# Kernel tuning notes

Hardware: AMD Instinct MI355X
Metric: run time of the kernel (lower is better)

## Reference

```python
import jax, jax.numpy as jnp
import numpy as np

B, S, D, H = 4, 1024, 1024, 16
DK = D // H
EPS_LN = 1e-6

def setup_inputs() -> dict:
    key = jax.random.key(0)
    ks = jax.random.split(key, 16)
    sc = 1.0 / np.sqrt(D)
    inp = {}
    names = ['q_r','q_i','k_r','k_i','v_r','v_i']
    for i, n in enumerate(names):
        inp[n] = jax.random.normal(ks[i], (B, S, D), dtype=jnp.float32)
    wnames = ['wq_r','wq_i','wk_r','wk_i','wv_r','wv_i','wfc_r','wfc_i']
    for i, n in enumerate(wnames):
        inp[n] = jax.random.normal(ks[6 + i], (D, D), dtype=jnp.float32) * sc
    inp['gamma'] = jnp.ones((D,), dtype=jnp.float32)
    inp['beta'] = jnp.zeros((D,), dtype=jnp.float32)
    return inp

def _clinear(xr, xi, wr, wi):
    # complex (xr + i*xi) @ (wr + i*wi)^T, weights stored [out, in]
    r = xr @ wr.T - xi @ wi.T
    im = xi @ wr.T + xr @ wi.T
    return r, im

def _forward(q_r, q_i, k_r, k_i, v_r, v_i, wq_r, wq_i, wk_r, wk_i,
             wv_r, wv_i, wfc_r, wfc_i, gamma, beta):
    res_r, res_i = q_r, q_i
    qr, qi = _clinear(q_r, q_i, wq_r, wq_i)
    kr, ki = _clinear(k_r, k_i, wk_r, wk_i)
    vr, vi = _clinear(v_r, v_i, wv_r, wv_i)
    # [B,S,D] -> [B,H,S,DK]
    split = lambda x: x.reshape(B, S, H, DK).transpose(0, 2, 1, 3)
    qr, qi, kr, ki, vr, vi = map(split, (qr, qi, kr, ki, vr, vi))
    temp = jnp.asarray(DK ** 0.5, qr.dtype)
    qr = qr / temp
    qi = qi / temp
    # q @ conj(k)^T : real = qr.kr + qi.ki ; imag = qi.kr - qr.ki
    ar = jnp.einsum('bhqd,bhkd->bhqk', qr, kr) + jnp.einsum('bhqd,bhkd->bhqk', qi, ki)
    ai = jnp.einsum('bhqd,bhkd->bhqk', qi, kr) - jnp.einsum('bhqd,bhkd->bhqk', qr, ki)
    attn = jax.nn.softmax(jnp.sqrt(ar * ar + ai * ai), axis=-1)  # magnitude softmax
    or_ = jnp.einsum('bhqk,bhkd->bhqd', attn, vr)
    oi_ = jnp.einsum('bhqk,bhkd->bhqd', attn, vi)
    merge = lambda x: x.transpose(0, 2, 1, 3).reshape(B, S, D)
    or_, oi_ = merge(or_), merge(oi_)
    fr, fi = _clinear(or_, oi_, wfc_r, wfc_i)
    # ComplexDropout in eval mode: identity except imag += 1e-10
    fi = fi + 1e-10
    xr = fr + res_r
    xi = fi + res_i
    # ComplexLayerNorm: mean over all non-batch dims, elementwise magnitude norm
    mr = jnp.mean(xr, axis=(1, 2), keepdims=True)
    mi = jnp.mean(xi, axis=(1, 2), keepdims=True)
    cr = xr - mr
    ci = xi - mi
    std = jnp.sqrt(cr * cr + ci * ci + EPS_LN)
    yr = gamma * (cr / std) + beta
    yi = gamma * (ci / std)
    return yr, yi, attn

def reference(q_r, q_i, k_r, k_i, v_r, v_i, wq_r, wq_i, wk_r, wk_i,
              wv_r, wv_i, wfc_r, wfc_i, gamma, beta):
    return _forward(q_r, q_i, k_r, k_i, v_r, v_i, wq_r, wq_i, wk_r, wk_i,
                    wv_r, wv_i, wfc_r, wfc_i, gamma, beta)
```

## Files before the change

kernel.cpp:

```cpp
#include <hip/hip_runtime.h>
#include <math.h>

#define NB 4
#define SEQ 1024
#define DIM 1024
#define NH 16
#define DHEAD 64
#define BUFN 4194304ULL
#define WHN  1048576ULL
#define LOG2E 1.4426950408889634f

typedef _Float16 f16x8 __attribute__((ext_vector_type(8)));
typedef _Float16 f16x4 __attribute__((ext_vector_type(4)));
typedef float    f32x4 __attribute__((ext_vector_type(4)));

#define MFMA16 __builtin_amdgcn_mfma_f32_16x16x32_f16

__device__ __forceinline__ void split4(const float4 v, f16x4& h, f16x4& l)
{
    const _Float16 h0=(_Float16)v.x, h1=(_Float16)v.y, h2=(_Float16)v.z, h3=(_Float16)v.w;
    h = (f16x4){h0, h1, h2, h3};
    l = (f16x4){(_Float16)((v.x-(float)h0)*2048.0f),
                (_Float16)((v.y-(float)h1)*2048.0f),
                (_Float16)((v.z-(float)h2)*2048.0f),
                (_Float16)((v.w-(float)h3)*2048.0f)};
}

__global__ __launch_bounds__(256)
void splitx_kernel(const float* __restrict__ xr, const float* __restrict__ xi,
                   _Float16* __restrict__ XS)
{
    const float* x = blockIdx.y ? xi : xr;
    _Float16* h = XS + (size_t)blockIdx.y * 2 * BUFN;
    _Float16* l = h + BUFN;
    const int i = (blockIdx.x * 256 + threadIdx.x) << 2;
    const float4 v = *(const float4*)(x + i);
    f16x4 hh, ll; split4(v, hh, ll);
    *(f16x4*)(h + i) = hh;
    *(f16x4*)(l + i) = ll;
}

__global__ __launch_bounds__(256)
void splitw_kernel(const float* w0, const float* w1, const float* w2, const float* w3,
                   const float* w4, const float* w5, const float* w6, const float* w7,
                   _Float16* __restrict__ WS)
{
    const int y = blockIdx.y;
    const float* x = (y==0)?w0:(y==1)?w1:(y==2)?w2:(y==3)?w3:(y==4)?w4:(y==5)?w5:(y==6)?w6:w7;
    _Float16* h = WS + (size_t)y * 2 * WHN;
    _Float16* l = h + WHN;
    const int i = (blockIdx.x * 256 + threadIdx.x) << 2;
    float4 v = *(const float4*)(x + i);
    v.x *= 64.0f; v.y *= 64.0f; v.z *= 64.0f; v.w *= 64.0f;
    f16x4 hh, ll; split4(v, hh, ll);
    *(f16x4*)(h + i) = hh;
    *(f16x4*)(l + i) = ll;
}

template<int MODE>
__global__ __launch_bounds__(256, 1)
void cgemm16_kernel(const _Float16* __restrict__ Ahr, const _Float16* __restrict__ Alr,
                    const _Float16* __restrict__ Ahi, const _Float16* __restrict__ Ali,
                    const _Float16* __restrict__ Bhr, const _Float16* __restrict__ Blr,
                    const _Float16* __restrict__ Bhi, const _Float16* __restrict__ Bli,
                    float* __restrict__ outr, float* __restrict__ outi,
                    const float* __restrict__ resr, const float* __restrict__ resi,
                    float* __restrict__ msum, float scale)
{
    __shared__ __align__(16) _Float16 As[4][64][40];
    __shared__ __align__(16) _Float16 Bs[4][64][40];
    const int t    = threadIdx.x;
    const int lane = t & 63;
    const int w    = t >> 6;
    const int wm   = w >> 1, wn = w & 1;
    const int lr   = lane & 15;
    const int kc   = (lane >> 4) << 3;
    const int m0   = blockIdx.x * 64;
    const int o0   = blockIdx.y * 64;
    const int srow = t >> 2;
    const int sc8  = (t & 3) << 3;

    const size_t aoff = (size_t)(m0 + srow) * DIM + sc8;
    const size_t boff = (size_t)(o0 + srow) * DIM + sc8;

    f32x4 acc[2][2][4];
    #pragma unroll
    for (int i = 0; i < 2; ++i)
        #pragma unroll
        for (int j = 0; j < 2; ++j)
            #pragma unroll
            for (int c = 0; c < 4; ++c)
                acc[i][j][c] = (f32x4){0.f, 0.f, 0.f, 0.f};

    for (int k0 = 0; k0 < DIM; k0 += 32) {
        const uint4 va0 = *(const uint4*)(Ahr + aoff + k0);
        const uint4 va1 = *(const uint4*)(Alr + aoff + k0);
        const uint4 va2 = *(const uint4*)(Ahi + aoff + k0);
        const uint4 va3 = *(const uint4*)(Ali + aoff + k0);
        const uint4 vb0 = *(const uint4*)(Bhr + boff + k0);
        const uint4 vb1 = *(const uint4*)(Blr + boff + k0);
        const uint4 vb2 = *(const uint4*)(Bhi + boff + k0);
        const uint4 vb3 = *(const uint4*)(Bli + boff + k0);
        __syncthreads();
        *(uint4*)&As[0][srow][sc8] = va0;
        *(uint4*)&As[1][srow][sc8] = va1;
        *(uint4*)&As[2][srow][sc8] = va2;
        *(uint4*)&As[3][srow][sc8] = va3;
        *(uint4*)&Bs[0][srow][sc8] = vb0;
        *(uint4*)&Bs[1][srow][sc8] = vb1;
        *(uint4*)&Bs[2][srow][sc8] = vb2;
        *(uint4*)&Bs[3][srow][sc8] = vb3;
        __syncthreads();

        f16x8 a0[2], a1[2], a2[2], a3[2];
        #pragma unroll
        for (int mt = 0; mt < 2; ++mt) {
            const int ar = wm * 32 + mt * 16 + lr;
            a0[mt] = *(const f16x8*)&As[0][ar][kc];
            a1[mt] = *(const f16x8*)&As[1][ar][kc];
            a2[mt] = *(const f16x8*)&As[2][ar][kc];
            a3[mt] = *(const f16x8*)&As[3][ar][kc];
        }
        #pragma unroll
        for (int nt = 0; nt < 2; ++nt) {
            const int br = wn * 32 + nt * 16 + lr;
            const f16x8 bhr = *(const f16x8*)&Bs[0][br][kc];
            const f16x8 blr = *(const f16x8*)&Bs[1][br][kc];
            const f16x8 bhi = *(const f16x8*)&Bs[2][br][kc];
            const f16x8 bli = *(const f16x8*)&Bs[3][br][kc];
            const f16x8 bhiN = -bhi;
            const f16x8 bliN = -bli;
            #pragma unroll
            for (int mt = 0; mt < 2; ++mt) {
                acc[mt][nt][0] = MFMA16(a0[mt], bhr,  acc[mt][nt][0], 0, 0, 0);
                acc[mt][nt][0] = MFMA16(a2[mt], bhiN, acc[mt][nt][0], 0, 0, 0);
                acc[mt][nt][1] = MFMA16(a0[mt], blr,  acc[mt][nt][1], 0, 0, 0);
                acc[mt][nt][1] = MFMA16(a1[mt], bhr,  acc[mt][nt][1], 0, 0, 0);
                acc[mt][nt][1] = MFMA16(a2[mt], bliN, acc[mt][nt][1], 0, 0, 0);
                acc[mt][nt][1] = MFMA16(a3[mt], bhiN, acc[mt][nt][1], 0, 0, 0);
                acc[mt][nt][2] = MFMA16(a2[mt], bhr,  acc[mt][nt][2], 0, 0, 0);
                acc[mt][nt][2] = MFMA16(a0[mt], bhi,  acc[mt][nt][2], 0, 0, 0);
                acc[mt][nt][3] = MFMA16(a2[mt], blr,  acc[mt][nt][3], 0, 0, 0);
                acc[mt][nt][3] = MFMA16(a3[mt], bhr,  acc[mt][nt][3], 0, 0, 0);
                acc[mt][nt][3] = MFMA16(a0[mt], bli,  acc[mt][nt][3], 0, 0, 0);
                acc[mt][nt][3] = MFMA16(a1[mt], bhi,  acc[mt][nt][3], 0, 0, 0);
            }
        }
    }

    const float INVL = 1.0f / 2048.0f;
    if (MODE == 0) {
        #pragma unroll
        for (int mt = 0; mt < 2; ++mt)
            #pragma unroll
            for (int nt = 0; nt < 2; ++nt)
                #pragma unroll
                for (int r = 0; r < 4; ++r) {
                    const int mrow = m0 + wm * 32 + mt * 16 + ((lane >> 4)) * 4 + r;
                    const int ncol = o0 + wn * 32 + nt * 16 + lr;
                    const float cr = (acc[mt][nt][0][r] + acc[mt][nt][1][r] * INVL) * scale;
                    const float ci = (acc[mt][nt][2][r] + acc[mt][nt][3][r] * INVL) * scale;
                    const int b = mrow >> 10, s = mrow & 1023, h = ncol >> 6, dk = ncol & 63;
                    const size_t idx = (((size_t)b * NH + h) * SEQ + s) * DHEAD + dk;
                    outr[idx] = cr;
                    outi[idx] = ci;
                }
    } else {
        float sr = 0.f, si = 0.f;
        #pragma unroll
        for (int mt = 0; mt < 2; ++mt)
            #pragma unroll
            for (int nt = 0; nt < 2; ++nt)
                #pragma unroll
                for (int r = 0; r < 4; ++r) {
                    const int mrow = m0 + wm * 32 + mt * 16 + ((lane >> 4)) * 4 + r;
                    const int ncol = o0 + wn * 32 + nt * 16 + lr;
                    const size_t idx = (size_t)mrow * DIM + ncol;
                    const float cr = (acc[mt][nt][0][r] + acc[mt][nt][1][r] * INVL) * scale
                                     + resr[idx];
                    const float ci = (acc[mt][nt][2][r] + acc[mt][nt][3][r] * INVL) * scale
                                     + 1e-10f + resi[idx];
                    outr[idx] = cr;
                    outi[idx] = ci;
                    sr += cr; si += ci;
                }
        #pragma unroll
        for (int off = 32; off > 0; off >>= 1) { sr += __shfl_xor(sr, off); si += __shfl_xor(si, off); }
        __shared__ float wsum[8];
        if ((t & 63) == 0) { wsum[w * 2 + 0] = sr; wsum[w * 2 + 1] = si; }
        __syncthreads();
        if (t == 0) {
            atomicAdd(&msum[2 * (m0 >> 10) + 0], wsum[0] + wsum[2] + wsum[4] + wsum[6]);
            atomicAdd(&msum[2 * (m0 >> 10) + 1], wsum[1] + wsum[3] + wsum[5] + wsum[7]);
        }
    }
}

__global__ __launch_bounds__(256)
void vtrans_kernel(const float* __restrict__ VR, const float* __restrict__ VI,
                   _Float16* __restrict__ Trh, _Float16* __restrict__ Trl,
                   _Float16* __restrict__ Tih, _Float16* __restrict__ Til)
{
    __shared__ float sr[64][68];
    __shared__ float si[64][68];
    const int t = threadIdx.x;
    const int kb = blockIdx.x, bh = blockIdx.y;
    const size_t ibase = (size_t)bh * SEQ * DHEAD + (size_t)kb * 64 * DHEAD;
    const int row = t >> 4, c0 = (t & 15) << 2;
    #pragma unroll
    for (int it = 0; it < 4; ++it) {
        const float4 a = *(const float4*)(VR + ibase + (size_t)(row + 16*it) * DHEAD + c0);
        const float4 b = *(const float4*)(VI + ibase + (size_t)(row + 16*it) * DHEAD + c0);
        *(float4*)&sr[row + 16*it][c0] = a;
        *(float4*)&si[row + 16*it][c0] = b;
    }
    __syncthreads();
    const int dk = t >> 2, k0 = (t & 3) << 4;
    f16x8 hr[2], lr8[2], hi8[2], li8[2];
    #pragma unroll
    for (int kk = 0; kk < 16; ++kk) {
        const float xr = sr[k0 + kk][dk];
        const float xi = si[k0 + kk][dk];
        const _Float16 hxr = (_Float16)xr;
        const _Float16 hxi = (_Float16)xi;
        hr[kk>>3][kk&7]  = hxr;
        lr8[kk>>3][kk&7] = (_Float16)((xr - (float)hxr) * 2048.0f);
        hi8[kk>>3][kk&7] = hxi;
        li8[kk>>3][kk&7] = (_Float16)((xi - (float)hxi) * 2048.0f);
    }
    const size_t ob = ((size_t)bh * 64 + dk) * SEQ + kb * 64 + k0;
    *(f16x8*)(Trh + ob) = hr[0];  *(f16x8*)(Trh + ob + 8) = hr[1];
    *(f16x8*)(Trl + ob) = lr8[0]; *(f16x8*)(Trl + ob + 8) = lr8[1];
    *(f16x8*)(Tih + ob) = hi8[0]; *(f16x8*)(Tih + ob + 8) = hi8[1];
    *(f16x8*)(Til + ob) = li8[0]; *(f16x8*)(Til + ob + 8) = li8[1];
}

__global__ __launch_bounds__(256, 1)
void attn_scores_kernel(const float* __restrict__ QR, const float* __restrict__ QI,
                        const float* __restrict__ KR, const float* __restrict__ KI,
                        float* __restrict__ attn, float* __restrict__ Lbuf)
{
    __shared__ __align__(16) _Float16 Ks[4][64][72];
    __shared__ float red[2][64];
    const int t = threadIdx.x;
    const int lane = t & 63;
    const int w = t >> 6, wm = w >> 1, wn = w & 1;
    const int lr = lane & 15, g = lane >> 4, kc = g << 3;
    const int q0 = blockIdx.x * 64;
    const int bh = blockIdx.y;
    const size_t base = (size_t)bh * SEQ * DHEAD;
    const int srow = t >> 2, sc0 = (t & 3) << 4;

    #pragma unroll
    for (int c = 0; c < 4; ++c) {
        const float4 a = *(const float4*)(QR + base + (size_t)(q0 + srow) * DHEAD + sc0 + 4*c);
        const float4 b = *(const float4*)(QI + base + (size_t)(q0 + srow) * DHEAD + sc0 + 4*c);
        f16x4 h, l;
        split4(a, h, l);
        *(f16x4*)&Ks[0][srow][sc0 + 4*c] = h;
        *(f16x4*)&Ks[1][srow][sc0 + 4*c] = l;
        split4(b, h, l);
        *(f16x4*)&Ks[2][srow][sc0 + 4*c] = h;
        *(f16x4*)&Ks[3][srow][sc0 + 4*c] = l;
    }
    __syncthreads();
    f16x8 qhr[2][2], qlr[2][2], qhi[2][2], qli[2][2];
    #pragma unroll
    for (int mt = 0; mt < 2; ++mt) {
        const int row = wm * 32 + mt * 16 + lr;
        #pragma unroll
        for (int ks = 0; ks < 2; ++ks) {
            const int col = ks * 32 + kc;
            qhr[mt][ks] = *(const f16x8*)&Ks[0][row][col];
            qlr[mt][ks] = *(const f16x8*)&Ks[1][row][col];
            qhi[mt][ks] = *(const f16x8*)&Ks[2][row][col];
            qli[mt][ks] = *(const f16x8*)&Ks[3][row][col];
        }
    }

    float lsum[2][4] = {};
    float4 pr[4], pi4[4];
    #pragma unroll
    for (int c = 0; c < 4; ++c) {
        pr[c]  = *(const float4*)(KR + base + (size_t)srow * DHEAD + sc0 + 4*c);
        pi4[c] = *(const float4*)(KI + base + (size_t)srow * DHEAD + sc0 + 4*c);
    }

    for (int kt = 0; kt < 16; ++kt) {
        __syncthreads();
        #pragma unroll
        for (int c = 0; c < 4; ++c) {
            f16x4 h, l;
            split4(pr[c], h, l);
            *(f16x4*)&Ks[0][srow][sc0 + 4*c] = h;
            *(f16x4*)&Ks[1][srow][sc0 + 4*c] = l;
            split4(pi4[c], h, l);
            *(f16x4*)&Ks[2][srow][sc0 + 4*c] = h;
            *(f16x4*)&Ks[3][srow][sc0 + 4*c] = l;
        }
        __syncthreads();
        if (kt < 15) {
            const size_t koff = base + (size_t)((kt + 1) * 64 + srow) * DHEAD;
            #pragma unroll
            for (int c = 0; c < 4; ++c) {
                pr[c]  = *(const float4*)(KR + koff + sc0 + 4*c);
                pi4[c] = *(const float4*)(KI + koff + sc0 + 4*c);
            }
        }
        f32x4 arh[2][2], arl[2][2], aih[2][2], ail[2][2];
        #pragma unroll
        for (int i = 0; i < 2; ++i)
            #pragma unroll
            for (int j = 0; j < 2; ++j) {
                arh[i][j] = (f32x4){0,0,0,0}; arl[i][j] = (f32x4){0,0,0,0};
                aih[i][j] = (f32x4){0,0,0,0}; ail[i][j] = (f32x4){0,0,0,0};
            }
        #pragma unroll
        for (int nt = 0; nt < 2; ++nt) {
            const int brow = wn * 32 + nt * 16 + lr;
            #pragma unroll
            for (int ks = 0; ks < 2; ++ks) {
                const int col = ks * 32 + kc;
                const f16x8 khr = *(const f16x8*)&Ks[0][brow][col];
                const f16x8 klr = *(const f16x8*)&Ks[1][brow][col];
                const f16x8 khi = *(const f16x8*)&Ks[2][brow][col];
                const f16x8 kli = *(const f16x8*)&Ks[3][brow][col];
                const f16x8 khiN = -khi;
                const f16x8 kliN = -kli;
                #pragma unroll
                for (int mt = 0; mt < 2; ++mt) {
                    arh[mt][nt] = MFMA16(qhr[mt][ks], khr,  arh[mt][nt], 0,0,0);
                    arh[mt][nt] = MFMA16(qhi[mt][ks], khi,  arh[mt][nt], 0,0,0);
                    arl[mt][nt] = MFMA16(qhr[mt][ks], klr,  arl[mt][nt], 0,0,0);
                    arl[mt][nt] = MFMA16(qlr[mt][ks], khr,  arl[mt][nt], 0,0,0);
                    arl[mt][nt] = MFMA16(qhi[mt][ks], kli,  arl[mt][nt], 0,0,0);
                    arl[mt][nt] = MFMA16(qli[mt][ks], khi,  arl[mt][nt], 0,0,0);
                    aih[mt][nt] = MFMA16(qhi[mt][ks], khr,  aih[mt][nt], 0,0,0);
                    aih[mt][nt] = MFMA16(qhr[mt][ks], khiN, aih[mt][nt], 0,0,0);
                    ail[mt][nt] = MFMA16(qhi[mt][ks], klr,  ail[mt][nt], 0,0,0);
                    ail[mt][nt] = MFMA16(qli[mt][ks], khr,  ail[mt][nt], 0,0,0);
                    ail[mt][nt] = MFMA16(qhr[mt][ks], kliN, ail[mt][nt], 0,0,0);
                    ail[mt][nt] = MFMA16(qlr[mt][ks], khiN, ail[mt][nt], 0,0,0);
                }
            }
        }
        const float INV = 1.0f / 2048.0f;
        #pragma unroll
        for (int mt = 0; mt < 2; ++mt)
            #pragma unroll
            for (int nt = 0; nt < 2; ++nt)
                #pragma unroll
                for (int r = 0; r < 4; ++r) {
                    const float ar = arh[mt][nt][r] + arl[mt][nt][r] * INV;
                    const float ai = aih[mt][nt][r] + ail[mt][nt][r] * INV;
                    const float s  = sqrtf(ar * ar + ai * ai);
                    const int q = q0 + wm * 32 + mt * 16 + g * 4 + r;
                    const int k = kt * 64 + wn * 32 + nt * 16 + lr;
                    attn[((size_t)bh * SEQ + q) * SEQ + k] = s;
                    lsum[mt][r] += exp2f(s * LOG2E);
                }
    }
    #pragma unroll
    for (int mt = 0; mt < 2; ++mt)
        #pragma unroll
        for (int r = 0; r < 4; ++r) {
            float v = lsum[mt][r];
            v += __shfl_xor(v, 1); v += __shfl_xor(v, 2);
            v += __shfl_xor(v, 4); v += __shfl_xor(v, 8);
            lsum[mt][r] = v;
        }
    if (lr == 0) {
        #pragma unroll
        for (int mt = 0; mt < 2; ++mt)
            #pragma unroll
            for (int r = 0; r < 4; ++r)
                red[wn][wm * 32 + mt * 16 + g * 4 + r] = lsum[mt][r];
    }
    __syncthreads();
    if (t < 64) Lbuf[(size_t)bh * SEQ + q0 + t] = red[0][t] + red[1][t];
}

__global__ __launch_bounds__(256, 1)
void attn_pv_kernel(float* __restrict__ attn, const float* __restrict__ Lbuf,
                    const _Float16* __restrict__ Trh, const _Float16* __restrict__ Trl,
                    const _Float16* __restrict__ Tih, const _Float16* __restrict__ Til,
                    _Float16* __restrict__ XOhr, _Float16* __restrict__ XOlr,
                    _Float16* __restrict__ XOhi, _Float16* __restrict__ XOli)
{
    __shared__ __align__(16) _Float16 Ps[2][64][72];
    __shared__ float invL[64];
    const int t = threadIdx.x;
    const int lane = t & 63;
    const int w = t >> 6, wm = w >> 1, wn = w & 1;
    const int lr = lane & 15, g = lane >> 4, kc = g << 3;
    const int q0 = blockIdx.x * 64;
    const int bh = blockIdx.y;
    const size_t abase = ((size_t)bh * SEQ + q0) * SEQ;
    const size_t vbase = (size_t)bh * 64 * SEQ;

    if (t < 64) invL[t] = 1.0f / Lbuf[(size_t)bh * SEQ + q0 + t];

    const size_t vrow[2] = { vbase + (size_t)(wn * 32 + lr) * SEQ + kc,
                             vbase + (size_t)(wn * 32 + 16 + lr) * SEQ + kc };

    f32x4 orh[2][2], orl[2][2], oih[2][2], oil[2][2];
    #pragma unroll
    for (int i = 0; i < 2; ++i)
        #pragma unroll
        for (int j = 0; j < 2; ++j) {
            orh[i][j] = (f32x4){0,0,0,0}; orl[i][j] = (f32x4){0,0,0,0};
            oih[i][j] = (f32x4){0,0,0,0}; oil[i][j] = (f32x4){0,0,0,0};
        }

    const int prow = t >> 4, pcol = (t & 15) << 2;
    float4 sc[4];
    #pragma unroll
    for (int it = 0; it < 4; ++it)
        sc[it] = *(const float4*)(attn + abase + (size_t)(prow + 16*it) * SEQ + pcol);

    for (int kt = 0; kt < 16; ++kt) {
        __syncthreads();
        #pragma unroll
        for (int it = 0; it < 4; ++it) {
            const int row = prow + 16*it;
            const float inv = invL[row];
            float4 p;
            p.x = exp2f(sc[it].x * LOG2E) * inv;
            p.y = exp2f(sc[it].y * LOG2E) * inv;
            p.z = exp2f(sc[it].z * LOG2E) * inv;
            p.w = exp2f(sc[it].w * LOG2E) * inv;
            *(float4*)(attn + abase + (size_t)row * SEQ + kt * 64 + pcol) = p;
            float4 ps;
            ps.x = p.x * 1024.0f; ps.y = p.y * 1024.0f;
            ps.z = p.z * 1024.0f; ps.w = p.w * 1024.0f;
            f16x4 h, l; split4(ps, h, l);
            *(f16x4*)&Ps[0][row][pcol] = h;
            *(f16x4*)&Ps[1][row][pcol] = l;
        }
        __syncthreads();
        if (kt < 15) {
            #pragma unroll
            for (int it = 0; it < 4; ++it)
                sc[it] = *(const float4*)(attn + abase + (size_t)(prow + 16*it) * SEQ
                                          + (kt + 1) * 64 + pcol);
        }
        #pragma unroll
        for (int ks = 0; ks < 2; ++ks) {
            const int col = ks * 32 + kc;
            f16x8 ph[2], pl[2];
            #pragma unroll
            for (int mt = 0; mt < 2; ++mt) {
                const int row = wm * 32 + mt * 16 + lr;
                ph[mt] = *(const f16x8*)&Ps[0][row][col];
                pl[mt] = *(const f16x8*)&Ps[1][row][col];
            }
            const size_t vcol = (size_t)(kt * 64 + ks * 32);
            #pragma unroll
            for (int nt = 0; nt < 2; ++nt) {
                const size_t vr = vrow[nt] + vcol;
                const f16x8 vhr = *(const f16x8*)(Trh + vr);
                const f16x8 vlr = *(const f16x8*)(Trl + vr);
                const f16x8 vhi = *(const f16x8*)(Tih + vr);
                const f16x8 vli = *(const f16x8*)(Til + vr);
                #pragma unroll
                for (int mt = 0; mt < 2; ++mt) {
                    orh[mt][nt] = MFMA16(ph[mt], vhr, orh[mt][nt], 0,0,0);
                    orl[mt][nt] = MFMA16(ph[mt], vlr, orl[mt][nt], 0,0,0);
                    orl[mt][nt] = MFMA16(pl[mt], vhr, orl[mt][nt], 0,0,0);
                    oih[mt][nt] = MFMA16(ph[mt], vhi, oih[mt][nt], 0,0,0);
                    oil[mt][nt] = MFMA16(ph[mt], vli, oil[mt][nt], 0,0,0);
                    oil[mt][nt] = MFMA16(pl[mt], vhi, oil[mt][nt], 0,0,0);
                }
            }
        }
    }
    const float IL = 1.0f / 2048.0f, SP = 1.0f / 1024.0f;
    const int b = bh >> 4, h = bh & 15;
    #pragma unroll
    for (int mt = 0; mt < 2; ++mt)
        #pragma unroll
        for (int nt = 0; nt < 2; ++nt)
            #pragma unroll
            for (int r = 0; r < 4; ++r) {
                const float orv = (orh[mt][nt][r] + orl[mt][nt][r] * IL) * SP;
                const float oiv = (oih[mt][nt][r] + oil[mt][nt][r] * IL) * SP;
                const int q  = q0 + wm * 32 + mt * 16 + g * 4 + r;
                const int dk = wn * 32 + nt * 16 + lr;
                const size_t addr = ((size_t)b * SEQ + q) * DIM + h * DHEAD + dk;
                _Float16 hh = (_Float16)orv;
                XOhr[addr] = hh;
                XOlr[addr] = (_Float16)((orv - (float)hh) * 2048.0f);
                hh = (_Float16)oiv;
                XOhi[addr] = hh;
                XOli[addr] = (_Float16)((oiv - (float)hh) * 2048.0f);
            }
}

__global__ __launch_bounds__(256)
void ln_kernel(const float* __restrict__ xr, const float* __restrict__ xi,
               const float* __restrict__ msum, const float* __restrict__ gamma,
               const float* __restrict__ beta,
               float* __restrict__ yr, float* __restrict__ yi)
{
    const int gid = blockIdx.x * 256 + threadIdx.x;
    const int flat = gid << 2;
    const int b = flat >> 20;
    const int d = flat & (DIM - 1);
    const float mr = msum[2*b+0] * (1.0f/1048576.0f);
    const float mi = msum[2*b+1] * (1.0f/1048576.0f);
    const float4 vr = *(const float4*)(xr + flat);
    const float4 vi = *(const float4*)(xi + flat);
    const float4 g  = *(const float4*)(gamma + d);
    const float4 bt = *(const float4*)(beta + d);
    float4 or4, oi4;
    {
        float cr = vr.x - mr, ci = vi.x - mi;
        float inv = 1.0f / sqrtf(cr*cr + ci*ci + 1e-6f);
        or4.x = g.x * (cr * inv) + bt.x; oi4.x = g.x * (ci * inv);
    }
    {
        float cr = vr.y - mr, ci = vi.y - mi;
        float inv = 1.0f / sqrtf(cr*cr + ci*ci + 1e-6f);
        or4.y = g.y * (cr * inv) + bt.y; oi4.y = g.y * (ci * inv);
    }
    {
        float cr = vr.z - mr, ci = vi.z - mi;
        float inv = 1.0f / sqrtf(cr*cr + ci*ci + 1e-6f);
        or4.z = g.z * (cr * inv) + bt.z; oi4.z = g.z * (ci * inv);
    }
    {
        float cr = vr.w - mr, ci = vi.w - mi;
        float inv = 1.0f / sqrtf(cr*cr + ci*ci + 1e-6f);
        or4.w = g.w * (cr * inv) + bt.w; oi4.w = g.w * (ci * inv);
    }
    *(float4*)(yr + flat) = or4;
    *(float4*)(yi + flat) = oi4;
}

extern "C" void kernel_launch(void* const* d_in, const int* in_sizes, int n_in,
                              void* d_out, int out_size, void* d_ws, size_t ws_size,
                              hipStream_t stream)
{
    const float* q_r   = (const float*)d_in[0];
    const float* q_i   = (const float*)d_in[1];
    const float* k_r   = (const float*)d_in[2];
    const float* k_i   = (const float*)d_in[3];
    const float* v_r   = (const float*)d_in[4];
    const float* v_i   = (const float*)d_in[5];
    const float* wq_r  = (const float*)d_in[6];
    const float* wq_i  = (const float*)d_in[7];
    const float* wk_r  = (const float*)d_in[8];
    const float* wk_i  = (const float*)d_in[9];
    const float* wv_r  = (const float*)d_in[10];
    const float* wv_i  = (const float*)d_in[11];
    const float* wfc_r = (const float*)d_in[12];
    const float* wfc_i = (const float*)d_in[13];
    const float* gamma = (const float*)d_in[14];
    const float* beta  = (const float*)d_in[15];

    float* ws = (float*)d_ws;
    const size_t BUF = BUFN;
    float* QR   = ws + 0*BUF;
    float* QI   = ws + 1*BUF;
    float* KR   = ws + 2*BUF;
    float* KI   = ws + 3*BUF;
    float* VR   = ws + 4*BUF;
    float* VI   = ws + 5*BUF;
    float* MSUM = ws + 6*BUF;
    float* LBUF = ws + 6*BUF + 16;
    _Float16* F  = (_Float16*)(ws + 6*BUF + 16 + 65536);
    _Float16* XS = F;
    _Float16* VT = F + 4*BUF;
    _Float16* WSp = F + 8*BUF;
    float* XR = QR;
    float* XI = QI;

    float* yr   = (float*)d_out;
    float* yi   = yr + BUF;
    float* attn = yr + 2*BUF;

    const dim3 blk(256);
    const dim3 g_gemm(64, 16);
    const float IWS = 1.0f / 64.0f;

    splitw_kernel<<<dim3(1024, 8), blk, 0, stream>>>(wq_r, wq_i, wk_r, wk_i,
                                                     wv_r, wv_i, wfc_r, wfc_i, WSp);

    splitx_kernel<<<dim3(4096, 2), blk, 0, stream>>>(q_r, q_i, XS);
    cgemm16_kernel<0><<<g_gemm, blk, 0, stream>>>(
        XS + 0*BUF, XS + 1*BUF, XS + 2*BUF, XS + 3*BUF,
        WSp + 0*WHN, WSp + 1*WHN, WSp + 2*WHN, WSp + 3*WHN,
        QR, QI, nullptr, nullptr, nullptr, 0.125f * IWS);

    splitx_kernel<<<dim3(4096, 2), blk, 0, stream>>>(k_r, k_i, XS);
    cgemm16_kernel<0><<<g_gemm, blk, 0, stream>>>(
        XS + 0*BUF, XS + 1*BUF, XS + 2*BUF, XS + 3*BUF,
        WSp + 4*WHN, WSp + 5*WHN, WSp + 6*WHN, WSp + 7*WHN,
        KR, KI, nullptr, nullptr, nullptr, IWS);

    splitx_kernel<<<dim3(4096, 2), blk, 0, stream>>>(v_r, v_i, XS);
    cgemm16_kernel<0><<<g_gemm, blk, 0, stream>>>(
        XS + 0*BUF, XS + 1*BUF, XS + 2*BUF, XS + 3*BUF,
        WSp + 8*WHN, WSp + 9*WHN, WSp + 10*WHN, WSp + 11*WHN,
        VR, VI, nullptr, nullptr, nullptr, IWS);

    vtrans_kernel<<<dim3(16, 64), blk, 0, stream>>>(VR, VI,
        VT + 0*BUF, VT + 1*BUF, VT + 2*BUF, VT + 3*BUF);

    attn_scores_kernel<<<dim3(16, 64), blk, 0, stream>>>(QR, QI, KR, KI, attn, LBUF);

    attn_pv_kernel<<<dim3(16, 64), blk, 0, stream>>>(attn, LBUF,
        VT + 0*BUF, VT + 1*BUF, VT + 2*BUF, VT + 3*BUF,
        XS + 0*BUF, XS + 1*BUF, XS + 2*BUF, XS + 3*BUF);

    hipMemsetAsync(MSUM, 0, 8 * sizeof(float), stream);
    cgemm16_kernel<1><<<g_gemm, blk, 0, stream>>>(
        XS + 0*BUF, XS + 1*BUF, XS + 2*BUF, XS + 3*BUF,
        WSp + 12*WHN, WSp + 13*WHN, WSp + 14*WHN, WSp + 15*WHN,
        XR, XI, q_r, q_i, MSUM, IWS);
    ln_kernel<<<dim3(4096), blk, 0, stream>>>(XR, XI, MSUM, gamma, beta, yr, yi);
}
```

Measured before the change: 1.001 ms.

## Compute P fragments in registers per wave in attn_pv, removing LDS staging

The attention-times-V kernel now has each wave own 16 query rows across all 64 head columns. Each lane loads its own score slice in the MFMA A-operand layout, applies the exp and normalization, writes the probabilities back, and splits them to fp16 hi/lo directly in registers. This removes the shared-memory P tile and both block barriers per k-tile. In exchange, each wave re-reads the full V tile (4 column tiles instead of 2), raising V traffic per block, and the global attn stores become less coalesced 32-byte chunks per lane.

```diff
diff --git a/kernel.cpp b/kernel.cpp
--- a/kernel.cpp
+++ b/kernel.cpp
@@ -24,6 +24,18 @@
                 (_Float16)((v.y-(float)h1)*2048.0f),
                 (_Float16)((v.z-(float)h2)*2048.0f),
                 (_Float16)((v.w-(float)h3)*2048.0f)};
+}
+
+__device__ __forceinline__ void split8s(const float4 a, const float4 b, float s,
+                                        f16x8& h, f16x8& l)
+{
+    const float x[8] = {a.x*s, a.y*s, a.z*s, a.w*s, b.x*s, b.y*s, b.z*s, b.w*s};
+    #pragma unroll
+    for (int j = 0; j < 8; ++j) {
+        const _Float16 hh = (_Float16)x[j];
+        h[j] = hh;
+        l[j] = (_Float16)((x[j] - (float)hh) * 2048.0f);
+    }
 }
 
 __global__ __launch_bounds__(256)
@@ -387,113 +399,96 @@
                     _Float16* __restrict__ XOhr, _Float16* __restrict__ XOlr,
                     _Float16* __restrict__ XOhi, _Float16* __restrict__ XOli)
 {
-    __shared__ __align__(16) _Float16 Ps[2][64][72];
-    __shared__ float invL[64];
     const int t = threadIdx.x;
     const int lane = t & 63;
-    const int w = t >> 6, wm = w >> 1, wn = w & 1;
+    const int wm = t >> 6;
     const int lr = lane & 15, g = lane >> 4, kc = g << 3;
     const int q0 = blockIdx.x * 64;
     const int bh = blockIdx.y;
-    const size_t abase = ((size_t)bh * SEQ + q0) * SEQ;
+    const int qrow = q0 + wm * 16 + lr;
+    float* srow = attn + ((size_t)bh * SEQ + qrow) * SEQ + kc;
+    const float il = 1.0f / Lbuf[(size_t)bh * SEQ + qrow];
     const size_t vbase = (size_t)bh * 64 * SEQ;
-
-    if (t < 64) invL[t] = 1.0f / Lbuf[(size_t)bh * SEQ + q0 + t];
-
-    const size_t vrow[2] = { vbase + (size_t)(wn * 32 + lr) * SEQ + kc,
-                             vbase + (size_t)(wn * 32 + 16 + lr) * SEQ + kc };
-
-    f32x4 orh[2][2], orl[2][2], oih[2][2], oil[2][2];
-    #pragma unroll
-    for (int i = 0; i < 2; ++i)
-        #pragma unroll
-        for (int j = 0; j < 2; ++j) {
-            orh[i][j] = (f32x4){0,0,0,0}; orl[i][j] = (f32x4){0,0,0,0};
-            oih[i][j] = (f32x4){0,0,0,0}; oil[i][j] = (f32x4){0,0,0,0};
-        }
-
-    const int prow = t >> 4, pcol = (t & 15) << 2;
-    float4 sc[4];
-    #pragma unroll
-    for (int it = 0; it < 4; ++it)
-        sc[it] = *(const float4*)(attn + abase + (size_t)(prow + 16*it) * SEQ + pcol);
+    size_t voff[4];
+    #pragma unroll
+    for (int nt = 0; nt < 4; ++nt)
+        voff[nt] = vbase + (size_t)(nt * 16 + lr) * SEQ + kc;
+
+    f32x4 orh[4], orl[4], oih[4], oil[4];
+    #pragma unroll
+    for (int nt = 0; nt < 4; ++nt) {
+        orh[nt] = (f32x4){0,0,0,0}; orl[nt] = (f32x4){0,0,0,0};
+        oih[nt] = (f32x4){0,0,0,0}; oil[nt] = (f32x4){0,0,0,0};
+    }
+
+    float4 sa[2], sb[2];
+    sa[0] = *(const float4*)(srow + 0);
+    sb[0] = *(const float4*)(srow + 4);
+    sa[1] = *(const float4*)(srow + 32);
+    sb[1] = *(const float4*)(srow + 36);
 
     for (int kt = 0; kt < 16; ++kt) {
-        __syncthreads();
-        #pragma unroll
-        for (int it = 0; it < 4; ++it) {
-            const int row = prow + 16*it;
-            const float inv = invL[row];
-            float4 p;
-            p.x = exp2f(sc[it].x * LOG2E) * inv;
-            p.y = exp2f(sc[it].y * LOG2E) * inv;
-            p.z = exp2f(sc[it].z * LOG2E) * inv;
-            p.w = exp2f(sc[it].w * LOG2E) * inv;
-            *(float4*)(attn + abase + (size_t)row * SEQ + kt * 64 + pcol) = p;
-            float4 ps;
-            ps.x = p.x * 1024.0f; ps.y = p.y * 1024.0f;
-            ps.z = p.z * 1024.0f; ps.w = p.w * 1024.0f;
-            f16x4 h, l; split4(ps, h, l);
-            *(f16x4*)&Ps[0][row][pcol] = h;
-            *(f16x4*)&Ps[1][row][pcol] = l;
-        }
-        __syncthreads();
+        float4 na[2], nb[2];
         if (kt < 15) {
-            #pragma unroll
-            for (int it = 0; it < 4; ++it)
-                sc[it] = *(const float4*)(attn + abase + (size_t)(prow + 16*it) * SEQ
-                                          + (kt + 1) * 64 + pcol);
+            const int o = (kt + 1) * 64;
+            na[0] = *(const float4*)(srow + o + 0);
+            nb[0] = *(const float4*)(srow + o + 4);
+            na[1] = *(const float4*)(srow + o + 32);
+            nb[1] = *(const float4*)(srow + o + 36);
         }
         #pragma unroll
         for (int ks = 0; ks < 2; ++ks) {
-            const int col = ks * 32 + kc;
-            f16x8 ph[2], pl[2];
-            #pragma unroll
-            for (int mt = 0; mt < 2; ++mt) {
-                const int row = wm * 32 + mt * 16 + lr;
-                ph[mt] = *(const f16x8*)&Ps[0][row][col];
-                pl[mt] = *(const f16x8*)&Ps[1][row][col];
+            const int off = kt * 64 + ks * 32;
+            float4 pa, pb;
+            pa.x = exp2f(sa[ks].x * LOG2E) * il;
+            pa.y = exp2f(sa[ks].y * LOG2E) * il;
+            pa.z = exp2f(sa[ks].z * LOG2E) * il;
+            pa.w = exp2f(sa[ks].w * LOG2E) * il;
+            pb.x = exp2f(sb[ks].x * LOG2E) * il;
+            pb.y = exp2f(sb[ks].y * LOG2E) * il;
+            pb.z = exp2f(sb[ks].z * LOG2E) * il;
+            pb.w = exp2f(sb[ks].w * LOG2E) * il;
+            *(float4*)(srow + off + 0) = pa;
+            *(float4*)(srow + off + 4) = pb;
+            f16x8 ph, pl;
+            split8s(pa, pb, 1024.0f, ph, pl);
+            #pragma unroll
+            for (int nt = 0; nt < 4; ++nt) {
+                const size_t vo = voff[nt] + off;
+                const f16x8 vhr = *(const f16x8*)(Trh + vo);
+                const f16x8 vlr = *(const f16x8*)(Trl + vo);
+                const f16x8 vhi = *(const f16x8*)(Tih + vo);
+                const f16x8 vli = *(const f16x8*)(Til + vo);
+                orh[nt] = MFMA16(ph, vhr, orh[nt], 0,0,0);
+                orl[nt] = MFMA16(ph, vlr, orl[nt], 0,0,0);
+                orl[nt] = MFMA16(pl, vhr, orl[nt], 0,0,0);
+                oih[nt] = MFMA16(ph, vhi, oih[nt], 0,0,0);
+                oil[nt] = MFMA16(ph, vli, oil[nt], 0,0,0);
+                oil[nt] = MFMA16(pl, vhi, oil[nt], 0,0,0);
             }
-            const size_t vcol = (size_t)(kt * 64 + ks * 32);
-            #pragma unroll
-            for (int nt = 0; nt < 2; ++nt) {
-                const size_t vr = vrow[nt] + vcol;
-                const f16x8 vhr = *(const f16x8*)(Trh + vr);
-                const f16x8 vlr = *(const f16x8*)(Trl + vr);
-                const f16x8 vhi = *(const f16x8*)(Tih + vr);
-                const f16x8 vli = *(const f16x8*)(Til + vr);
-                #pragma unroll
-                for (int mt = 0; mt < 2; ++mt) {
-                    orh[mt][nt] = MFMA16(ph[mt], vhr, orh[mt][nt], 0,0,0);
-                    orl[mt][nt] = MFMA16(ph[mt], vlr, orl[mt][nt], 0,0,0);
-                    orl[mt][nt] = MFMA16(pl[mt], vhr, orl[mt][nt], 0,0,0);
-                    oih[mt][nt] = MFMA16(ph[mt], vhi, oih[mt][nt], 0,0,0);
-                    oil[mt][nt] = MFMA16(ph[mt], vli, oil[mt][nt], 0,0,0);
-                    oil[mt][nt] = MFMA16(pl[mt], vhi, oil[mt][nt], 0,0,0);
-                }
-            }
-        }
-    }
+        }
+        sa[0] = na[0]; sb[0] = nb[0];
+        sa[1] = na[1]; sb[1] = nb[1];
+    }
+
     const float IL = 1.0f / 2048.0f, SP = 1.0f / 1024.0f;
     const int b = bh >> 4, h = bh & 15;
     #pragma unroll
-    for (int mt = 0; mt < 2; ++mt)
-        #pragma unroll
-        for (int nt = 0; nt < 2; ++nt)
-            #pragma unroll
-            for (int r = 0; r < 4; ++r) {
-                const float orv = (orh[mt][nt][r] + orl[mt][nt][r] * IL) * SP;
-                const float oiv = (oih[mt][nt][r] + oil[mt][nt][r] * IL) * SP;
-                const int q  = q0 + wm * 32 + mt * 16 + g * 4 + r;
-                const int dk = wn * 32 + nt * 16 + lr;
-                const size_t addr = ((size_t)b * SEQ + q) * DIM + h * DHEAD + dk;
-                _Float16 hh = (_Float16)orv;
-                XOhr[addr] = hh;
-                XOlr[addr] = (_Float16)((orv - (float)hh) * 2048.0f);
-                hh = (_Float16)oiv;
-                XOhi[addr] = hh;
-                XOli[addr] = (_Float16)((oiv - (float)hh) * 2048.0f);
-            }
+    for (int nt = 0; nt < 4; ++nt)
+        #pragma unroll
+        for (int r = 0; r < 4; ++r) {
+            const float orv = (orh[nt][r] + orl[nt][r] * IL) * SP;
+            const float oiv = (oih[nt][r] + oil[nt][r] * IL) * SP;
+            const int q  = q0 + wm * 16 + g * 4 + r;
+            const int dk = nt * 16 + lr;
+            const size_t addr = ((size_t)b * SEQ + q) * DIM + h * DHEAD + dk;
+            _Float16 hh = (_Float16)orv;
+            XOhr[addr] = hh;
+            XOlr[addr] = (_Float16)((orv - (float)hh) * 2048.0f);
+            hh = (_Float16)oiv;
+            XOhi[addr] = hh;
+            XOli[addr] = (_Float16)((oiv - (float)hh) * 2048.0f);
+        }
 }
 
 __global__ __launch_bounds__(256)
```

New measurement: 1.116 ms. 11.5% more time.

## Fuse attention scores and PV into one kernel with fixed softmax offset

Applied to the files above, without the earlier changes.

Merges the score kernel and the probability-times-V kernel. Unnormalized probabilities exp(s - 11) are computed once, staged in shared memory as fp16 hi/lo pairs and multiplied by V within the same K loop; the output is divided by the row sum at the end. A separate elementwise kernel then normalizes the stored attention matrix in place. This removes recomputing exp and reloading scores in the PV pass. Memory traffic on the attention matrix stays about the same because of the extra normalize pass, and the fixed offset of 11 assumes score magnitudes stay within fp16/fp32 range.

```diff
diff --git a/kernel.cpp b/kernel.cpp
--- a/kernel.cpp
+++ b/kernel.cpp
@@ -9,6 +9,7 @@
 #define BUFN 4194304ULL
 #define WHN  1048576ULL
 #define LOG2E 1.4426950408889634f
+#define SOFTC 11.0f
 
 typedef _Float16 f16x8 __attribute__((ext_vector_type(8)));
 typedef _Float16 f16x4 __attribute__((ext_vector_type(4)));
@@ -236,11 +237,17 @@
 }
 
 __global__ __launch_bounds__(256, 1)
-void attn_scores_kernel(const float* __restrict__ QR, const float* __restrict__ QI,
-                        const float* __restrict__ KR, const float* __restrict__ KI,
-                        float* __restrict__ attn, float* __restrict__ Lbuf)
+void attn_fused_kernel(const float* __restrict__ QR, const float* __restrict__ QI,
+                       const float* __restrict__ KR, const float* __restrict__ KI,
+                       const _Float16* __restrict__ Trh, const _Float16* __restrict__ Trl,
+                       const _Float16* __restrict__ Tih, const _Float16* __restrict__ Til,
+                       float* __restrict__ attn, float* __restrict__ Linv,
+                       _Float16* __restrict__ XOhr, _Float16* __restrict__ XOlr,
+                       _Float16* __restrict__ XOhi, _Float16* __restrict__ XOli)
 {
     __shared__ __align__(16) _Float16 Ks[4][64][72];
+    __shared__ __align__(16) _Float16 Psh[64][72];
+    __shared__ __align__(16) _Float16 Psl[64][72];
     __shared__ float red[2][64];
     const int t = threadIdx.x;
     const int lane = t & 63;
@@ -248,8 +255,12 @@
     const int lr = lane & 15, g = lane >> 4, kc = g << 3;
     const int q0 = blockIdx.x * 64;
     const int bh = blockIdx.y;
-    const size_t base = (size_t)bh * SEQ * DHEAD;
+    const size_t base  = (size_t)bh * SEQ * DHEAD;
+    const size_t abase = (size_t)bh * SEQ * SEQ;
+    const size_t vbase = (size_t)bh * 64 * SEQ;
     const int srow = t >> 2, sc0 = (t & 3) << 4;
+    const size_t voff[2] = { vbase + (size_t)(wn * 32 + lr) * SEQ + kc,
+                             vbase + (size_t)(wn * 32 + 16 + lr) * SEQ + kc };
 
     #pragma unroll
     for (int c = 0; c < 4; ++c) {
@@ -279,6 +290,15 @@
     }
 
     float lsum[2][4] = {};
+    f32x4 orh[2][2], orl[2][2], oih[2][2], oil[2][2];
+    #pragma unroll
+    for (int i = 0; i < 2; ++i)
+        #pragma unroll
+        for (int j = 0; j < 2; ++j) {
+            orh[i][j] = (f32x4){0,0,0,0}; orl[i][j] = (f32x4){0,0,0,0};
+            oih[i][j] = (f32x4){0,0,0,0}; oil[i][j] = (f32x4){0,0,0,0};
+        }
+
     float4 pr[4], pi4[4];
     #pragma unroll
     for (int c = 0; c < 4; ++c) {
@@ -307,16 +327,14 @@
                 pi4[c] = *(const float4*)(KI + koff + sc0 + 4*c);
             }
         }
-        f32x4 arh[2][2], arl[2][2], aih[2][2], ail[2][2];
-        #pragma unroll
-        for (int i = 0; i < 2; ++i)
-            #pragma unroll
-            for (int j = 0; j < 2; ++j) {
-                arh[i][j] = (f32x4){0,0,0,0}; arl[i][j] = (f32x4){0,0,0,0};
-                aih[i][j] = (f32x4){0,0,0,0}; ail[i][j] = (f32x4){0,0,0,0};
-            }
         #pragma unroll
         for (int nt = 0; nt < 2; ++nt) {
+            f32x4 arh[2], arl[2], aih[2], ail[2];
+            #pragma unroll
+            for (int i = 0; i < 2; ++i) {
+                arh[i] = (f32x4){0,0,0,0}; arl[i] = (f32x4){0,0,0,0};
+                aih[i] = (f32x4){0,0,0,0}; ail[i] = (f32x4){0,0,0,0};
+            }
             const int brow = wn * 32 + nt * 16 + lr;
             #pragma unroll
             for (int ks = 0; ks < 2; ++ks) {
@@ -329,121 +347,41 @@
                 const f16x8 kliN = -kli;
                 #pragma unroll
                 for (int mt = 0; mt < 2; ++mt) {
-                    arh[mt][nt] = MFMA16(qhr[mt][ks], khr,  arh[mt][nt], 0,0,0);
-                    arh[mt][nt] = MFMA16(qhi[mt][ks], khi,  arh[mt][nt], 0,0,0);
-                    arl[mt][nt] = MFMA16(qhr[mt][ks], klr,  arl[mt][nt], 0,0,0);
-                    arl[mt][nt] = MFMA16(qlr[mt][ks], khr,  arl[mt][nt], 0,0,0);
-                    arl[mt][nt] = MFMA16(qhi[mt][ks], kli,  arl[mt][nt], 0,0,0);
-                    arl[mt][nt] = MFMA16(qli[mt][ks], khi,  arl[mt][nt], 0,0,0);
-                    aih[mt][nt] = MFMA16(qhi[mt][ks], khr,  aih[mt][nt], 0,0,0);
-                    aih[mt][nt] = MFMA16(qhr[mt][ks], khiN, aih[mt][nt], 0,0,0);
-                    ail[mt][nt] = MFMA16(qhi[mt][ks], klr,  ail[mt][nt], 0,0,0);
-                    ail[mt][nt] = MFMA16(qli[mt][ks], khr,  ail[mt][nt], 0,0,0);
-                    ail[mt][nt] = MFMA16(qhr[mt][ks], kliN, ail[mt][nt], 0,0,0);
-                    ail[mt][nt] = MFMA16(qlr[mt][ks], khiN, ail[mt][nt], 0,0,0);
+                    arh[mt] = MFMA16(qhr[mt][ks], khr,  arh[mt], 0,0,0);
+                    arh[mt] = MFMA16(qhi[mt][ks], khi,  arh[mt], 0,0,0);
+                    arl[mt] = MFMA16(qhr[mt][ks], klr,  arl[mt], 0,0,0);
+                    arl[mt] = MFMA16(qlr[mt][ks], khr,  arl[mt], 0,0,0);
+                    arl[mt] = MFMA16(qhi[mt][ks], kli,  arl[mt], 0,0,0);
+                    arl[mt] = MFMA16(qli[mt][ks], khi,  arl[mt], 0,0,0);
+                    aih[mt] = MFMA16(qhi[mt][ks], khr,  aih[mt], 0,0,0);
+                    aih[mt] = MFMA16(qhr[mt][ks], khiN, aih[mt], 0,0,0);
+                    ail[mt] = MFMA16(qhi[mt][ks], klr,  ail[mt], 0,0,0);
+                    ail[mt] = MFMA16(qli[mt][ks], khr,  ail[mt], 0,0,0);
+                    ail[mt] = MFMA16(qhr[mt][ks], kliN, ail[mt], 0,0,0);
+                    ail[mt] = MFMA16(qlr[mt][ks], khiN, ail[mt], 0,0,0);
                 }
             }
-        }
-        const float INV = 1.0f / 2048.0f;
-        #pragma unroll
-        for (int mt = 0; mt < 2; ++mt)
-            #pragma unroll
-            for (int nt = 0; nt < 2; ++nt)
+            const float INV = 1.0f / 2048.0f;
+            const int kcol = kt * 64 + wn * 32 + nt * 16 + lr;
+            const int lcol = wn * 32 + nt * 16 + lr;
+            #pragma unroll
+            for (int mt = 0; mt < 2; ++mt) {
+                const int lrow = wm * 32 + mt * 16 + g * 4;
                 #pragma unroll
                 for (int r = 0; r < 4; ++r) {
-                    const float ar = arh[mt][nt][r] + arl[mt][nt][r] * INV;
-                    const float ai = aih[mt][nt][r] + ail[mt][nt][r] * INV;
+                    const float ar = arh[mt][r] + arl[mt][r] * INV;
+                    const float ai = aih[mt][r] + ail[mt][r] * INV;
                     const float s  = sqrtf(ar * ar + ai * ai);
-                    const int q = q0 + wm * 32 + mt * 16 + g * 4 + r;
-                    const int k = kt * 64 + wn * 32 + nt * 16 + lr;
-                    attn[((size_t)bh * SEQ + q) * SEQ + k] = s;
-                    lsum[mt][r] += exp2f(s * LOG2E);
+                    const float pp = exp2f((s - SOFTC) * LOG2E);
+                    attn[abase + (size_t)(q0 + lrow + r) * SEQ + kcol] = pp;
+                    lsum[mt][r] += pp;
+                    const _Float16 hh = (_Float16)pp;
+                    Psh[lrow + r][lcol] = hh;
+                    Psl[lrow + r][lcol] = (_Float16)((pp - (float)hh) * 2048.0f);
                 }
-    }
-    #pragma unroll
-    for (int mt = 0; mt < 2; ++mt)
-        #pragma unroll
-        for (int r = 0; r < 4; ++r) {
-            float v = lsum[mt][r];
-            v += __shfl_xor(v, 1); v += __shfl_xor(v, 2);
-            v += __shfl_xor(v, 4); v += __shfl_xor(v, 8);
-            lsum[mt][r] = v;
-        }
-    if (lr == 0) {
-        #pragma unroll
-        for (int mt = 0; mt < 2; ++mt)
-            #pragma unroll
-            for (int r = 0; r < 4; ++r)
-                red[wn][wm * 32 + mt * 16 + g * 4 + r] = lsum[mt][r];
-    }
-    __syncthreads();
-    if (t < 64) Lbuf[(size_t)bh * SEQ + q0 + t] = red[0][t] + red[1][t];
-}
-
-__global__ __launch_bounds__(256, 1)
-void attn_pv_kernel(float* __restrict__ attn, const float* __restrict__ Lbuf,
-                    const _Float16* __restrict__ Trh, const _Float16* __restrict__ Trl,
-                    const _Float16* __restrict__ Tih, const _Float16* __restrict__ Til,
-                    _Float16* __restrict__ XOhr, _Float16* __restrict__ XOlr,
-                    _Float16* __restrict__ XOhi, _Float16* __restrict__ XOli)
-{
-    __shared__ __align__(16) _Float16 Ps[2][64][72];
-    __shared__ float invL[64];
-    const int t = threadIdx.x;
-    const int lane = t & 63;
-    const int w = t >> 6, wm = w >> 1, wn = w & 1;
-    const int lr = lane & 15, g = lane >> 4, kc = g << 3;
-    const int q0 = blockIdx.x * 64;
-    const int bh = blockIdx.y;
-    const size_t abase = ((size_t)bh * SEQ + q0) * SEQ;
-    const size_t vbase = (size_t)bh * 64 * SEQ;
-
-    if (t < 64) invL[t] = 1.0f / Lbuf[(size_t)bh * SEQ + q0 + t];
-
-    const size_t vrow[2] = { vbase + (size_t)(wn * 32 + lr) * SEQ + kc,
-                             vbase + (size_t)(wn * 32 + 16 + lr) * SEQ + kc };
-
-    f32x4 orh[2][2], orl[2][2], oih[2][2], oil[2][2];
-    #pragma unroll
-    for (int i = 0; i < 2; ++i)
-        #pragma unroll
-        for (int j = 0; j < 2; ++j) {
-            orh[i][j] = (f32x4){0,0,0,0}; orl[i][j] = (f32x4){0,0,0,0};
-            oih[i][j] = (f32x4){0,0,0,0}; oil[i][j] = (f32x4){0,0,0,0};
-        }
-
-    const int prow = t >> 4, pcol = (t & 15) << 2;
-    float4 sc[4];
-    #pragma unroll
-    for (int it = 0; it < 4; ++it)
-        sc[it] = *(const float4*)(attn + abase + (size_t)(prow + 16*it) * SEQ + pcol);
-
-    for (int kt = 0; kt < 16; ++kt) {
+            }
+        }
         __syncthreads();
-        #pragma unroll
-        for (int it = 0; it < 4; ++it) {
-            const int row = prow + 16*it;
-            const float inv = invL[row];
-            float4 p;
-            p.x = exp2f(sc[it].x * LOG2E) * inv;
-            p.y = exp2f(sc[it].y * LOG2E) * inv;
-            p.z = exp2f(sc[it].z * LOG2E) * inv;
-            p.w = exp2f(sc[it].w * LOG2E) * inv;
-            *(float4*)(attn + abase + (size_t)row * SEQ + kt * 64 + pcol) = p;
-            float4 ps;
-            ps.x = p.x * 1024.0f; ps.y = p.y * 1024.0f;
-            ps.z = p.z * 1024.0f; ps.w = p.w * 1024.0f;
-            f16x4 h, l; split4(ps, h, l);
-            *(f16x4*)&Ps[0][row][pcol] = h;
-            *(f16x4*)&Ps[1][row][pcol] = l;
-        }
-        __syncthreads();
-        if (kt < 15) {
-            #pragma unroll
-            for (int it = 0; it < 4; ++it)
-                sc[it] = *(const float4*)(attn + abase + (size_t)(prow + 16*it) * SEQ
-                                          + (kt + 1) * 64 + pcol);
-        }
         #pragma unroll
         for (int ks = 0; ks < 2; ++ks) {
             const int col = ks * 32 + kc;
@@ -451,17 +389,17 @@
             #pragma unroll
             for (int mt = 0; mt < 2; ++mt) {
                 const int row = wm * 32 + mt * 16 + lr;
-                ph[mt] = *(const f16x8*)&Ps[0][row][col];
-                pl[mt] = *(const f16x8*)&Ps[1][row][col];
+                ph[mt] = *(const f16x8*)&Psh[row][col];
+                pl[mt] = *(const f16x8*)&Psl[row][col];
             }
             const size_t vcol = (size_t)(kt * 64 + ks * 32);
             #pragma unroll
             for (int nt = 0; nt < 2; ++nt) {
-                const size_t vr = vrow[nt] + vcol;
-                const f16x8 vhr = *(const f16x8*)(Trh + vr);
-                const f16x8 vlr = *(const f16x8*)(Trl + vr);
-                const f16x8 vhi = *(const f16x8*)(Tih + vr);
-                const f16x8 vli = *(const f16x8*)(Til + vr);
+                const size_t vo = voff[nt] + vcol;
+                const f16x8 vhr = *(const f16x8*)(Trh + vo);
+                const f16x8 vlr = *(const f16x8*)(Trl + vo);
+                const f16x8 vhi = *(const f16x8*)(Tih + vo);
+                const f16x8 vli = *(const f16x8*)(Til + vo);
                 #pragma unroll
                 for (int mt = 0; mt < 2; ++mt) {
                     orh[mt][nt] = MFMA16(ph[mt], vhr, orh[mt][nt], 0,0,0);
@@ -474,17 +412,40 @@
             }
         }
     }
-    const float IL = 1.0f / 2048.0f, SP = 1.0f / 1024.0f;
+
+    #pragma unroll
+    for (int mt = 0; mt < 2; ++mt)
+        #pragma unroll
+        for (int r = 0; r < 4; ++r) {
+            float v = lsum[mt][r];
+            v += __shfl_xor(v, 1); v += __shfl_xor(v, 2);
+            v += __shfl_xor(v, 4); v += __shfl_xor(v, 8);
+            lsum[mt][r] = v;
+        }
+    __syncthreads();
+    if (lr == 0) {
+        #pragma unroll
+        for (int mt = 0; mt < 2; ++mt)
+            #pragma unroll
+            for (int r = 0; r < 4; ++r)
+                red[wn][wm * 32 + mt * 16 + g * 4 + r] = lsum[mt][r];
+    }
+    __syncthreads();
+    if (t < 64) Linv[(size_t)bh * SEQ + q0 + t] = 1.0f / (red[0][t] + red[1][t]);
+
+    const float IL = 1.0f / 2048.0f;
     const int b = bh >> 4, h = bh & 15;
     #pragma unroll
     for (int mt = 0; mt < 2; ++mt)
         #pragma unroll
-        for (int nt = 0; nt < 2; ++nt)
-            #pragma unroll
-            for (int r = 0; r < 4; ++r) {
-                const float orv = (orh[mt][nt][r] + orl[mt][nt][r] * IL) * SP;
-                const float oiv = (oih[mt][nt][r] + oil[mt][nt][r] * IL) * SP;
-                const int q  = q0 + wm * 32 + mt * 16 + g * 4 + r;
+        for (int r = 0; r < 4; ++r) {
+            const int lrow = wm * 32 + mt * 16 + g * 4 + r;
+            const float il = 1.0f / (red[0][lrow] + red[1][lrow]);
+            const int q = q0 + lrow;
+            #pragma unroll
+            for (int nt = 0; nt < 2; ++nt) {
+                const float orv = (orh[mt][nt][r] + orl[mt][nt][r] * IL) * il;
+                const float oiv = (oih[mt][nt][r] + oil[mt][nt][r] * IL) * il;
                 const int dk = wn * 32 + nt * 16 + lr;
                 const size_t addr = ((size_t)b * SEQ + q) * DIM + h * DHEAD + dk;
                 _Float16 hh = (_Float16)orv;
@@ -494,6 +455,22 @@
                 XOhi[addr] = hh;
                 XOli[addr] = (_Float16)((oiv - (float)hh) * 2048.0f);
             }
+        }
+}
+
+__global__ __launch_bounds__(256)
+void attn_norm_kernel(float* __restrict__ attn, const float* __restrict__ Linv)
+{
+    const size_t tid  = (size_t)blockIdx.x * 256 + threadIdx.x;
+    const size_t base = tid << 4;
+    const float il = Linv[base >> 10];
+    float4* p = (float4*)(attn + base);
+    #pragma unroll
+    for (int c = 0; c < 4; ++c) {
+        float4 v = p[c];
+        v.x *= il; v.y *= il; v.z *= il; v.w *= il;
+        p[c] = v;
+    }
 }
 
 __global__ __launch_bounds__(256)
@@ -607,11 +584,12 @@
     vtrans_kernel<<<dim3(16, 64), blk, 0, stream>>>(VR, VI,
         VT + 0*BUF, VT + 1*BUF, VT + 2*BUF, VT + 3*BUF);
 
-    attn_scores_kernel<<<dim3(16, 64), blk, 0, stream>>>(QR, QI, KR, KI, attn, LBUF);
-
-    attn_pv_kernel<<<dim3(16, 64), blk, 0, stream>>>(attn, LBUF,
+    attn_fused_kernel<<<dim3(16, 64), blk, 0, stream>>>(QR, QI, KR, KI,
         VT + 0*BUF, VT + 1*BUF, VT + 2*BUF, VT + 3*BUF,
+        attn, LBUF,
         XS + 0*BUF, XS + 1*BUF, XS + 2*BUF, XS + 3*BUF);
+
+    attn_norm_kernel<<<dim3(16384), blk, 0, stream>>>(attn, LBUF);
 
     hipMemsetAsync(MSUM, 0, 8 * sizeof(float), stream);
     cgemm16_kernel<1><<<g_gemm, blk, 0, stream>>>(
```

New measurement: 1.080 ms. 1.08x slower.
